# Kernel optimization log

Hardware: AMD Instinct MI355X
Metric: run time of the kernel (lower is better)

The kernel has to match this reference:

```python
import jax, jax.numpy as jnp
import numpy as np

B, S, MAX_K, MID, V = 4, 512, 32, 32, 32000


def _lin(x, W, b):
    # torch nn.Linear convention: W is [out, in]
    return x @ W.T + b


def _label_count_segment(vals):
    """Distinct-label counts over prefixes [0:1],[0:2],...,[0:K] of the kNN labels."""
    Bv, Sv, K = vals.shape
    mask = jnp.triu(jnp.ones((K, K), dtype=bool), k=1)  # [K,K], True above diagonal
    # row i of expand keeps labels [0:i+1], rest filled with -1 (as in masked_fill)
    ev = jnp.where(mask, jnp.array(-1, vals.dtype), vals[:, :, None, :])  # [B,S,K,K]
    s = jnp.sort(ev, axis=-1)
    # zero-out adjacent duplicates (keep first occurrence)
    dedup = jnp.concatenate([s[..., :1], s[..., 1:] * (s[..., 1:] != s[..., :-1])], axis=-1)
    cnt = (dedup != 0).sum(-1)  # [B,S,K]
    cnt = cnt.at[..., :-1].add(-1)  # remove the single surviving -1 for rows 0..K-2
    return cnt


def setup_inputs():
    key = jax.random.key(0)
    ks = jax.random.split(key, 16)
    tgt_index = jax.random.randint(ks[0], (B, S, MAX_K), 0, V)
    knn_dists = jax.random.uniform(ks[1], (B, S, MAX_K), jnp.float32, 1e-3, 10.0)
    knn_key_feature = jax.random.uniform(ks[2], (B, S, MAX_K), jnp.float32, 1e-4, 1.0)
    network_probs = jax.random.uniform(ks[3], (B, S, V), jnp.float32, 1e-6, 1.0)
    network_probs = network_probs / network_probs.sum(-1, keepdims=True)
    network_select_probs = jax.random.uniform(ks[4], (B, S, MAX_K), jnp.float32, 1e-6, 1e-2)
    init = lambda k, shape: 0.02 * jax.random.normal(k, shape, jnp.float32)
    return {
        "tgt_index": tgt_index,
        "knn_dists": knn_dists,
        "knn_key_feature": knn_key_feature,
        "network_probs": network_probs,
        "network_select_probs": network_select_probs,
        # distance_func: Linear(2K+8, 1)
        "W_func": init(ks[5], (1, 2 * MAX_K + 8)), "b_func": init(ks[6], (1,)),
        # distance_fc1: Linear(2,4) -> Tanh -> Linear(4,1)
        "W1a": init(ks[7], (4, 2)), "b1a": init(ks[8], (4,)),
        "W1b": init(ks[9], (1, 4)), "b1b": init(ks[10], (1,)),
        # distance_fc2: Linear(2K, mid) -> Tanh -> Linear(mid, 2)
        "W2a": init(ks[11], (MID, 2 * MAX_K)), "b2a": init(ks[12], (MID,)),
        "W2b": init(ks[13], (2, MID)), "b2b": init(ks[14], (2,)),
    }


def reference(tgt_index, knn_dists, knn_key_feature, network_probs, network_select_probs,
              W_func, b_func, W1a, b1a, W1b, b1b, W2a, b2a, W2b, b2b):
    Bv, Sv, K = knn_dists.shape
    Vv = network_probs.shape[-1]
    label_counts = _label_count_segment(tgt_index)  # [B,S,K] int
    log_key = jnp.log(knn_key_feature)
    log_sel = jnp.log(network_select_probs)
    all_key_feature = jnp.stack([log_key, log_sel], axis=-1)  # [B,S,K,2]
    top_prob, _ = jax.lax.top_k(network_probs, 8)  # [B,S,8]
    knn_feat = jnp.concatenate([knn_dists, label_counts.astype(knn_dists.dtype)], -1)  # [B,S,2K]
    noise_logit = _lin(jnp.tanh(_lin(all_key_feature, W1a, b1a)), W1b, b1b).squeeze(-1)  # [B,S,K]
    sim_in = jnp.concatenate([jnp.log(top_prob), log_key, log_sel], -1)  # [B,S,2K+8]
    sim_lambda = _lin(sim_in, W_func, b_func)  # [B,S,1]
    lambda_logit = _lin(jnp.tanh(_lin(knn_feat, W2a, b2a)), W2b, b2b)  # [B,S,2]
    knn_lambda = jax.nn.softmax(jnp.concatenate([lambda_logit[..., :1], sim_lambda], -1), -1)[..., :1]
    tempe = jax.nn.sigmoid(lambda_logit[..., 1:2])  # [B,S,1]
    probs = jax.nn.softmax(-knn_dists * tempe + noise_logit, -1)  # [B,S,K]
    bi = jnp.arange(Bv)[:, None, None]
    si = jnp.arange(Sv)[None, :, None]
    knn_prob = jnp.zeros((Bv, Sv, Vv), probs.dtype).at[bi, si, tgt_index].set(probs)
    return knn_prob, knn_lambda
```

## Files before the change

### kernel.cpp

```cpp
#include <hip/hip_runtime.h>

typedef unsigned long long ull;
typedef float f4 __attribute__((ext_vector_type(4)));

#define TOKENS 2048
#define KNN    32
#define VOCAB  32000
#define CAP    512

#define INSK(key) do {                                                       \
    ull k_ = (key);                                                          \
    if (k_ > c7) {                                                           \
        ull tmp_;                                                            \
        if (k_ > c0) { tmp_ = c0; c0 = k_; k_ = tmp_; }                      \
        if (k_ > c1) { tmp_ = c1; c1 = k_; k_ = tmp_; }                      \
        if (k_ > c2) { tmp_ = c2; c2 = k_; k_ = tmp_; }                      \
        if (k_ > c3) { tmp_ = c3; c3 = k_; k_ = tmp_; }                      \
        if (k_ > c4) { tmp_ = c4; c4 = k_; k_ = tmp_; }                      \
        if (k_ > c5) { tmp_ = c5; c5 = k_; k_ = tmp_; }                      \
        if (k_ > c6) { tmp_ = c6; c6 = k_; k_ = tmp_; }                      \
        c7 = (k_ > c7) ? k_ : c7;                                            \
    }                                                                        \
} while (0)

#define INSF(vv) do {                                                        \
    float x_ = (vv);                                                         \
    if (x_ > t7) {                                                           \
        float h_;                                                            \
        h_ = fmaxf(t0, x_); x_ = fminf(t0, x_); t0 = h_;                     \
        h_ = fmaxf(t1, x_); x_ = fminf(t1, x_); t1 = h_;                     \
        h_ = fmaxf(t2, x_); x_ = fminf(t2, x_); t2 = h_;                     \
        h_ = fmaxf(t3, x_); x_ = fminf(t3, x_); t3 = h_;                     \
        h_ = fmaxf(t4, x_); x_ = fminf(t4, x_); t4 = h_;                     \
        h_ = fmaxf(t5, x_); x_ = fminf(t5, x_); t5 = h_;                     \
        h_ = fmaxf(t6, x_); x_ = fminf(t6, x_); t6 = h_;                     \
        t7 = fmaxf(t7, x_);                                                  \
    }                                                                        \
} while (0)

#define MAX4(v_) fmaxf(fmaxf(v_.x, v_.y), fmaxf(v_.z, v_.w))

#define COLLECT(v_) do {                                                     \
    if (v_.x >= T) { int p = atomicAdd(&s_n, 1); if (p < CAP) s_cand[p] = v_.x; } \
    if (v_.y >= T) { int p = atomicAdd(&s_n, 1); if (p < CAP) s_cand[p] = v_.y; } \
    if (v_.z >= T) { int p = atomicAdd(&s_n, 1); if (p < CAP) s_cand[p] = v_.z; } \
    if (v_.w >= T) { int p = atomicAdd(&s_n, 1); if (p < CAP) s_cand[p] = v_.w; } \
} while (0)

#define BATCH8(kb) do {                                                      \
    f4 v0 = np4[tid + (((kb)+0) << 8)];                                      \
    f4 v1 = np4[tid + (((kb)+1) << 8)];                                      \
    f4 v2 = np4[tid + (((kb)+2) << 8)];                                      \
    f4 v3 = np4[tid + (((kb)+3) << 8)];                                      \
    f4 v4 = np4[tid + (((kb)+4) << 8)];                                      \
    f4 v5 = np4[tid + (((kb)+5) << 8)];                                      \
    f4 v6 = np4[tid + (((kb)+6) << 8)];                                      \
    f4 v7 = np4[tid + (((kb)+7) << 8)];                                      \
    float m01 = fmaxf(MAX4(v0), MAX4(v1));                                   \
    float m23 = fmaxf(MAX4(v2), MAX4(v3));                                   \
    float m45 = fmaxf(MAX4(v4), MAX4(v5));                                   \
    float m67 = fmaxf(MAX4(v6), MAX4(v7));                                   \
    m = fmaxf(m, fmaxf(fmaxf(m01, m23), fmaxf(m45, m67)));                   \
} while (0)

__global__ __launch_bounds__(256, 8)
void k_scan(const float* __restrict__ net_probs, float* __restrict__ ws)
{
    const int t   = blockIdx.x;
    const int tid = threadIdx.x;

    __shared__ float s_max[256];
    __shared__ float s_cand[CAP];
    __shared__ int   s_n;
    __shared__ float s_thr;
    __shared__ float s_top8[8];

    if (tid == 0) s_n = 0;

    const f4* np4 = (const f4*)(net_probs + (size_t)t * VOCAB);

    float m = 0.f;
    BATCH8(0);
    BATCH8(8);
    BATCH8(16);
    {
        f4 v0 = np4[tid + (24 << 8)];
        f4 v1 = np4[tid + (25 << 8)];
        f4 v2 = np4[tid + (26 << 8)];
        f4 v3 = np4[tid + (27 << 8)];
        f4 v4 = np4[tid + (28 << 8)];
        f4 v5 = np4[tid + (29 << 8)];
        f4 v6 = np4[tid + (30 << 8)];
        float m01 = fmaxf(MAX4(v0), MAX4(v1));
        float m23 = fmaxf(MAX4(v2), MAX4(v3));
        float m45 = fmaxf(MAX4(v4), MAX4(v5));
        m = fmaxf(m, fmaxf(fmaxf(m01, m23), fmaxf(m45, MAX4(v6))));
    }
    if (tid < 64) {
        f4 v = np4[tid + (31 << 8)];
        m = fmaxf(m, MAX4(v));
    }
    s_max[tid] = m;
    __syncthreads();

    if (tid < 64) {
        ull c0 = 0, c1 = 0, c2 = 0, c3 = 0, c4 = 0, c5 = 0, c6 = 0, c7 = 0;
        #pragma unroll
        for (int k = 0; k < 4; ++k) {
            int idx = tid + (k << 6);
            ull key = (((ull)__float_as_uint(s_max[idx])) << 32) | (unsigned)idx;
            INSK(key);
        }
        ull g = 0;
        for (int r = 0; r < 8; ++r) {
            g = c0;
            #pragma unroll
            for (int off = 1; off < 64; off <<= 1) {
                ull o = __shfl_xor(g, off);
                if (o > g) g = o;
            }
            if (c0 == g) {
                c0 = c1; c1 = c2; c2 = c3; c3 = c4; c4 = c5; c5 = c6; c6 = c7; c7 = 0;
            }
        }
        if (tid == 0) s_thr = __uint_as_float((unsigned)(g >> 32));
    }
    __syncthreads();
    const float T = s_thr;

    if (m >= T) {
        for (int k = 0; k < 31; ++k) {
            f4 v = np4[tid + (k << 8)];
            COLLECT(v);
        }
        if (tid < 64) {
            f4 v = np4[tid + (31 << 8)];
            COLLECT(v);
        }
    }
    __syncthreads();
    const int n = s_n;

    if (n <= CAP) {
        if (tid < 64) {
            ull c0 = 0, c1 = 0, c2 = 0, c3 = 0, c4 = 0, c5 = 0, c6 = 0, c7 = 0;
            for (int i = tid; i < n; i += 64) {
                ull key = (((ull)__float_as_uint(s_cand[i])) << 32) | (unsigned)i;
                INSK(key);
            }
            for (int r = 0; r < 8; ++r) {
                ull g = c0;
                #pragma unroll
                for (int off = 1; off < 64; off <<= 1) {
                    ull o = __shfl_xor(g, off);
                    if (o > g) g = o;
                }
                if (c0 == g && g != 0ULL) {
                    c0 = c1; c1 = c2; c2 = c3; c3 = c4; c4 = c5; c5 = c6; c6 = c7; c7 = 0;
                }
                if (tid == 0) s_top8[r] = __uint_as_float((unsigned)(g >> 32));
            }
        }
    } else {
        float t0 = 0.f, t1 = 0.f, t2 = 0.f, t3 = 0.f,
              t4 = 0.f, t5 = 0.f, t6 = 0.f, t7 = 0.f;
        for (int k = 0; k < 31; ++k) {
            f4 v = np4[tid + (k << 8)];
            if (MAX4(v) > t7) { INSF(v.x); INSF(v.y); INSF(v.z); INSF(v.w); }
        }
        if (tid < 64) {
            f4 v = np4[tid + (31 << 8)];
            if (MAX4(v) > t7) { INSF(v.x); INSF(v.y); INSF(v.z); INSF(v.w); }
        }
        for (int r = 0; r < 8; ++r) {
            s_max[tid] = t0;
            __syncthreads();
            if (tid < 64) {
                float g = s_max[tid];
                g = fmaxf(g, s_max[tid + 64]);
                g = fmaxf(g, s_max[tid + 128]);
                g = fmaxf(g, s_max[tid + 192]);
                #pragma unroll
                for (int off = 1; off < 64; off <<= 1)
                    g = fmaxf(g, __shfl_xor(g, off));
                if (tid == 0) { s_thr = g; s_top8[r] = g; }
            }
            __syncthreads();
            float g = s_thr;
            ull mask = __ballot(t0 == g);
            __shared__ int s_win;
            if (tid == 0) s_win = 0x7fffffff;
            __syncthreads();
            if (t0 == g) atomicMin(&s_win, tid);
            __syncthreads();
            if (tid == s_win) {
                t0 = t1; t1 = t2; t2 = t3; t3 = t4; t4 = t5; t5 = t6; t6 = t7; t7 = 0.f;
            }
            __syncthreads();
            (void)mask;
        }
    }
    __syncthreads();

    if (tid < 8) ws[(size_t)t * 8 + tid] = s_top8[tid];
}

__global__ __launch_bounds__(256, 8)
void k_zero(float* __restrict__ out)
{
    const int t   = blockIdx.x;
    const int tid = threadIdx.x;
    f4*      o4 = (f4*)(out + (size_t)t * VOCAB);
    const f4 z4 = (f4){0.f, 0.f, 0.f, 0.f};
    #pragma unroll
    for (int k = 0; k < 31; ++k) o4[tid + (k << 8)] = z4;
    if (tid < 64) o4[tid + (31 << 8)] = z4;
}

__global__ __launch_bounds__(256, 8)
void k2_final(const int*   __restrict__ tgt_index,
              const float* __restrict__ knn_dists,
              const float* __restrict__ knn_key,
              const float* __restrict__ net_sel,
              const float* __restrict__ W_func, const float* __restrict__ b_func,
              const float* __restrict__ W1a,    const float* __restrict__ b1a,
              const float* __restrict__ W1b,    const float* __restrict__ b1b,
              const float* __restrict__ W2a,    const float* __restrict__ b2a,
              const float* __restrict__ W2b,    const float* __restrict__ b2b,
              const float* __restrict__ ws,
              float* __restrict__ out)
{
    const int t   = blockIdx.x;
    const int tid = threadIdx.x;

    __shared__ int   s_tgt[KNN];
    __shared__ float s_dist[KNN];
    __shared__ float s_cnt[KNN];
    __shared__ float s_top8[8];

    int   tg = 0;
    float d = 0.f, lk = 0.f, ls = 0.f;
    if (tid < KNN) {
        tg = tgt_index[t * KNN + tid];
        d  = knn_dists[t * KNN + tid];
        lk = logf(knn_key[t * KNN + tid]);
        ls = logf(net_sel[t * KNN + tid]);
        s_tgt[tid]  = tg;
        s_dist[tid] = d;
    }
    if (tid < 8) s_top8[tid] = ws[(size_t)t * 8 + tid];
    __syncthreads();

    if (tid < KNN) {
        int fo = (tg != 0) ? 1 : 0;
        if (fo) {
            for (int j = 0; j < tid; ++j)
                if (s_tgt[j] == tg) { fo = 0; break; }
        }
        int c = fo;
        #pragma unroll
        for (int off = 1; off < KNN; off <<= 1) {
            int n2 = __shfl_up(c, off, KNN);
            if (tid >= off) c += n2;
        }
        s_cnt[tid] = (float)c;
    }
    __syncthreads();

    if (tid < KNN) {
        float noise = b1b[0];
        #pragma unroll
        for (int j = 0; j < 4; ++j) {
            float z = tanhf(W1a[2 * j] * lk + W1a[2 * j + 1] * ls + b1a[j]);
            noise += W1b[j] * z;
        }

        float sp = W_func[8 + tid] * lk + W_func[40 + tid] * ls;
        if (tid < 8) sp += W_func[tid] * logf(s_top8[tid]);
        #pragma unroll
        for (int off = 16; off; off >>= 1) sp += __shfl_xor(sp, off, KNN);
        float sim = sp + b_func[0];

        float h = b2a[tid];
        const float* wr = W2a + tid * 64;
        #pragma unroll 8
        for (int i = 0; i < KNN; ++i) h += wr[i] * s_dist[i];
        #pragma unroll 8
        for (int i = 0; i < KNN; ++i) h += wr[KNN + i] * s_cnt[i];
        h = tanhf(h);
        float p0 = W2b[tid] * h;
        float p1 = W2b[KNN + tid] * h;
        #pragma unroll
        for (int off = 16; off; off >>= 1) {
            p0 += __shfl_xor(p0, off, KNN);
            p1 += __shfl_xor(p1, off, KNN);
        }
        float l0 = p0 + b2b[0];
        float l1 = p1 + b2b[1];

        float tempe = 1.f / (1.f + expf(-l1));
        float lam   = 1.f / (1.f + expf(-(l0 - sim)));

        float logit = -d * tempe + noise;
        float mx = logit;
        #pragma unroll
        for (int off = 16; off; off >>= 1) mx = fmaxf(mx, __shfl_xor(mx, off, KNN));
        float e = expf(logit - mx);
        float se = e;
        #pragma unroll
        for (int off = 16; off; off >>= 1) se += __shfl_xor(se, off, KNN);
        float p = e / se;

        bool wrte = true;
        for (int j = tid + 1; j < KNN; ++j)
            if (s_tgt[j] == tg) { wrte = false; break; }
        if (wrte) out[(size_t)t * VOCAB + tg] = p;

        if (tid == 0) out[(size_t)TOKENS * VOCAB + t] = lam;
    }
}

extern "C" void kernel_launch(void* const* d_in, const int* in_sizes, int n_in,
                              void* d_out, int out_size, void* d_ws, size_t ws_size,
                              hipStream_t stream) {
    float* ws = (float*)d_ws;

    k_scan<<<TOKENS, 256, 0, stream>>>((const float*)d_in[3], ws);
    k_zero<<<TOKENS, 256, 0, stream>>>((float*)d_out);
    k2_final<<<TOKENS, 256, 0, stream>>>(
        (const int*)  d_in[0],
        (const float*)d_in[1],
        (const float*)d_in[2],
        (const float*)d_in[4],
        (const float*)d_in[5],  (const float*)d_in[6],
        (const float*)d_in[7],  (const float*)d_in[8],
        (const float*)d_in[9],  (const float*)d_in[10],
        (const float*)d_in[11], (const float*)d_in[12],
        (const float*)d_in[13], (const float*)d_in[14],
        ws,
        (float*)d_out);
}
```

Baseline: 147.1 us.

## Split top-8 into flat segment-max pass and fused candidate gather in final kernel

The per-token scan kernel is replaced by a flat streaming kernel that computes the max of each 256-float segment (one wavefront, 125 segments per token) and writes those to the workspace. The top-8 selection then moves into the final kernel: it derives a threshold from the top segment maxima, re-reads only the qualifying segments, and collects candidates in shared memory. The zero-fill kernel also becomes a flat grid-stride pattern. This removes the full second per-token pass and the separate top-k kernel, at the cost of heavier shared-memory use in the final kernel and a dependence on exact segment-to-token alignment.

```diff
diff --git a/kernel.cpp b/kernel.cpp
--- a/kernel.cpp
+++ b/kernel.cpp
@@ -6,7 +6,14 @@
 #define TOKENS 2048
 #define KNN    32
 #define VOCAB  32000
-#define CAP    512
+#define NB_STREAM 2000
+#define NT_STREAM (NB_STREAM * 256)
+#define ITER      32
+#define NWAVE     (NT_STREAM / 64)
+#define SEG_PER_TOK 125
+#define CAP    2048
+
+#define MAX4(v_) fmaxf(fmaxf(v_.x, v_.y), fmaxf(v_.z, v_.w))
 
 #define INSK(key) do {                                                       \
     ull k_ = (key);                                                          \
@@ -38,8 +45,6 @@
     }                                                                        \
 } while (0)
 
-#define MAX4(v_) fmaxf(fmaxf(v_.x, v_.y), fmaxf(v_.z, v_.w))
-
 #define COLLECT(v_) do {                                                     \
     if (v_.x >= T) { int p = atomicAdd(&s_n, 1); if (p < CAP) s_cand[p] = v_.x; } \
     if (v_.y >= T) { int p = atomicAdd(&s_n, 1); if (p < CAP) s_cand[p] = v_.y; } \
@@ -47,70 +52,84 @@
     if (v_.w >= T) { int p = atomicAdd(&s_n, 1); if (p < CAP) s_cand[p] = v_.w; } \
 } while (0)
 
-#define BATCH8(kb) do {                                                      \
-    f4 v0 = np4[tid + (((kb)+0) << 8)];                                      \
-    f4 v1 = np4[tid + (((kb)+1) << 8)];                                      \
-    f4 v2 = np4[tid + (((kb)+2) << 8)];                                      \
-    f4 v3 = np4[tid + (((kb)+3) << 8)];                                      \
-    f4 v4 = np4[tid + (((kb)+4) << 8)];                                      \
-    f4 v5 = np4[tid + (((kb)+5) << 8)];                                      \
-    f4 v6 = np4[tid + (((kb)+6) << 8)];                                      \
-    f4 v7 = np4[tid + (((kb)+7) << 8)];                                      \
-    float m01 = fmaxf(MAX4(v0), MAX4(v1));                                   \
-    float m23 = fmaxf(MAX4(v2), MAX4(v3));                                   \
-    float m45 = fmaxf(MAX4(v4), MAX4(v5));                                   \
-    float m67 = fmaxf(MAX4(v6), MAX4(v7));                                   \
-    m = fmaxf(m, fmaxf(fmaxf(m01, m23), fmaxf(m45, m67)));                   \
-} while (0)
-
 __global__ __launch_bounds__(256, 8)
-void k_scan(const float* __restrict__ net_probs, float* __restrict__ ws)
+void k1_segmax(const float* __restrict__ net_probs, float* __restrict__ ws)
+{
+    const int g = blockIdx.x * 256 + threadIdx.x;
+    const int w = g >> 6;
+    const f4* np4 = (const f4*)net_probs;
+    #pragma unroll 4
+    for (int i = 0; i < ITER; ++i) {
+        f4 v = np4[(size_t)g + (size_t)i * NT_STREAM];
+        float m = MAX4(v);
+        #pragma unroll
+        for (int off = 32; off; off >>= 1) m = fmaxf(m, __shfl_xor(m, off));
+        if ((threadIdx.x & 63) == 0) ws[w + i * NWAVE] = m;
+    }
+}
+
+__global__ __launch_bounds__(256, 8)
+void k_zero(float* __restrict__ out)
+{
+    const int g = blockIdx.x * 256 + threadIdx.x;
+    f4* o4 = (f4*)out;
+    const f4 z4 = (f4){0.f, 0.f, 0.f, 0.f};
+    #pragma unroll 8
+    for (int i = 0; i < ITER; ++i)
+        o4[(size_t)g + (size_t)i * NT_STREAM] = z4;
+}
+
+__global__ __launch_bounds__(256, 8)
+void k2_final(const int*   __restrict__ tgt_index,
+              const float* __restrict__ knn_dists,
+              const float* __restrict__ knn_key,
+              const float* __restrict__ net_probs,
+              const float* __restrict__ net_sel,
+              const float* __restrict__ W_func, const float* __restrict__ b_func,
+              const float* __restrict__ W1a,    const float* __restrict__ b1a,
+              const float* __restrict__ W1b,    const float* __restrict__ b1b,
+              const float* __restrict__ W2a,    const float* __restrict__ b2a,
+              const float* __restrict__ W2b,    const float* __restrict__ b2b,
+              const float* __restrict__ ws,
+              float* __restrict__ out)
 {
     const int t   = blockIdx.x;
     const int tid = threadIdx.x;
 
-    __shared__ float s_max[256];
+    __shared__ float s_sm[128];
+    __shared__ int   s_qseg[128];
+    __shared__ int   s_nq;
+    __shared__ float s_thr;
     __shared__ float s_cand[CAP];
     __shared__ int   s_n;
-    __shared__ float s_thr;
+    __shared__ float s_red[256];
+    __shared__ int   s_win;
+    __shared__ int   s_tgt[KNN];
+    __shared__ float s_dist[KNN];
+    __shared__ float s_cnt[KNN];
     __shared__ float s_top8[8];
 
-    if (tid == 0) s_n = 0;
-
-    const f4* np4 = (const f4*)(net_probs + (size_t)t * VOCAB);
-
-    float m = 0.f;
-    BATCH8(0);
-    BATCH8(8);
-    BATCH8(16);
-    {
-        f4 v0 = np4[tid + (24 << 8)];
-        f4 v1 = np4[tid + (25 << 8)];
-        f4 v2 = np4[tid + (26 << 8)];
-        f4 v3 = np4[tid + (27 << 8)];
-        f4 v4 = np4[tid + (28 << 8)];
-        f4 v5 = np4[tid + (29 << 8)];
-        f4 v6 = np4[tid + (30 << 8)];
-        float m01 = fmaxf(MAX4(v0), MAX4(v1));
-        float m23 = fmaxf(MAX4(v2), MAX4(v3));
-        float m45 = fmaxf(MAX4(v4), MAX4(v5));
-        m = fmaxf(m, fmaxf(fmaxf(m01, m23), fmaxf(m45, MAX4(v6))));
-    }
-    if (tid < 64) {
-        f4 v = np4[tid + (31 << 8)];
-        m = fmaxf(m, MAX4(v));
-    }
-    s_max[tid] = m;
+    if (tid == 0) { s_nq = 0; s_n = 0; }
+
+    int   tg = 0;
+    float d = 0.f, lk = 0.f, ls = 0.f;
+    if (tid < KNN) {
+        tg = tgt_index[t * KNN + tid];
+        d  = knn_dists[t * KNN + tid];
+        lk = logf(knn_key[t * KNN + tid]);
+        ls = logf(net_sel[t * KNN + tid]);
+        s_tgt[tid]  = tg;
+        s_dist[tid] = d;
+    }
+    if (tid < 128) s_sm[tid] = (tid < SEG_PER_TOK) ? ws[t * SEG_PER_TOK + tid] : 0.f;
     __syncthreads();
 
     if (tid < 64) {
         ull c0 = 0, c1 = 0, c2 = 0, c3 = 0, c4 = 0, c5 = 0, c6 = 0, c7 = 0;
-        #pragma unroll
-        for (int k = 0; k < 4; ++k) {
-            int idx = tid + (k << 6);
-            ull key = (((ull)__float_as_uint(s_max[idx])) << 32) | (unsigned)idx;
-            INSK(key);
-        }
+        ull k0 = (((ull)__float_as_uint(s_sm[tid])) << 32) | (unsigned)tid;
+        INSK(k0);
+        ull k1 = (((ull)__float_as_uint(s_sm[tid + 64])) << 32) | (unsigned)(tid + 64);
+        INSK(k1);
         ull g = 0;
         for (int r = 0; r < 8; ++r) {
             g = c0;
@@ -128,13 +147,19 @@
     __syncthreads();
     const float T = s_thr;
 
-    if (m >= T) {
-        for (int k = 0; k < 31; ++k) {
-            f4 v = np4[tid + (k << 8)];
-            COLLECT(v);
-        }
-        if (tid < 64) {
-            f4 v = np4[tid + (31 << 8)];
+    if (tid < SEG_PER_TOK && s_sm[tid] >= T) {
+        int p = atomicAdd(&s_nq, 1);
+        s_qseg[p] = tid;
+    }
+    __syncthreads();
+    const int nq = s_nq;
+
+    const f4* np4 = (const f4*)(net_probs + (size_t)t * VOCAB);
+    for (int base = 0; base < nq; base += 4) {
+        int qi = base + (tid >> 6);
+        if (qi < nq) {
+            int seg = s_qseg[qi];
+            f4 v = np4[seg * 64 + (tid & 63)];
             COLLECT(v);
         }
     }
@@ -173,82 +198,28 @@
             if (MAX4(v) > t7) { INSF(v.x); INSF(v.y); INSF(v.z); INSF(v.w); }
         }
         for (int r = 0; r < 8; ++r) {
-            s_max[tid] = t0;
+            s_red[tid] = t0;
             __syncthreads();
             if (tid < 64) {
-                float g = s_max[tid];
-                g = fmaxf(g, s_max[tid + 64]);
-                g = fmaxf(g, s_max[tid + 128]);
-                g = fmaxf(g, s_max[tid + 192]);
+                float g = s_red[tid];
+                g = fmaxf(g, s_red[tid + 64]);
+                g = fmaxf(g, s_red[tid + 128]);
+                g = fmaxf(g, s_red[tid + 192]);
                 #pragma unroll
                 for (int off = 1; off < 64; off <<= 1)
                     g = fmaxf(g, __shfl_xor(g, off));
                 if (tid == 0) { s_thr = g; s_top8[r] = g; }
             }
-            __syncthreads();
-            float g = s_thr;
-            ull mask = __ballot(t0 == g);
-            __shared__ int s_win;
             if (tid == 0) s_win = 0x7fffffff;
             __syncthreads();
-            if (t0 == g) atomicMin(&s_win, tid);
+            if (t0 == s_thr) atomicMin(&s_win, tid);
             __syncthreads();
             if (tid == s_win) {
                 t0 = t1; t1 = t2; t2 = t3; t3 = t4; t4 = t5; t5 = t6; t6 = t7; t7 = 0.f;
             }
             __syncthreads();
-            (void)mask;
-        }
-    }
-    __syncthreads();
-
-    if (tid < 8) ws[(size_t)t * 8 + tid] = s_top8[tid];
-}
-
-__global__ __launch_bounds__(256, 8)
-void k_zero(float* __restrict__ out)
-{
-    const int t   = blockIdx.x;
-    const int tid = threadIdx.x;
-    f4*      o4 = (f4*)(out + (size_t)t * VOCAB);
-    const f4 z4 = (f4){0.f, 0.f, 0.f, 0.f};
-    #pragma unroll
-    for (int k = 0; k < 31; ++k) o4[tid + (k << 8)] = z4;
-    if (tid < 64) o4[tid + (31 << 8)] = z4;
-}
-
-__global__ __launch_bounds__(256, 8)
-void k2_final(const int*   __restrict__ tgt_index,
-              const float* __restrict__ knn_dists,
-              const float* __restrict__ knn_key,
-              const float* __restrict__ net_sel,
-              const float* __restrict__ W_func, const float* __restrict__ b_func,
-              const float* __restrict__ W1a,    const float* __restrict__ b1a,
-              const float* __restrict__ W1b,    const float* __restrict__ b1b,
-              const float* __restrict__ W2a,    const float* __restrict__ b2a,
-              const float* __restrict__ W2b,    const float* __restrict__ b2b,
-              const float* __restrict__ ws,
-              float* __restrict__ out)
-{
-    const int t   = blockIdx.x;
-    const int tid = threadIdx.x;
-
-    __shared__ int   s_tgt[KNN];
-    __shared__ float s_dist[KNN];
-    __shared__ float s_cnt[KNN];
-    __shared__ float s_top8[8];
-
-    int   tg = 0;
-    float d = 0.f, lk = 0.f, ls = 0.f;
-    if (tid < KNN) {
-        tg = tgt_index[t * KNN + tid];
-        d  = knn_dists[t * KNN + tid];
-        lk = logf(knn_key[t * KNN + tid]);
-        ls = logf(net_sel[t * KNN + tid]);
-        s_tgt[tid]  = tg;
-        s_dist[tid] = d;
-    }
-    if (tid < 8) s_top8[tid] = ws[(size_t)t * 8 + tid];
+        }
+    }
     __syncthreads();
 
     if (tid < KNN) {
@@ -325,12 +296,13 @@
                               hipStream_t stream) {
     float* ws = (float*)d_ws;
 
-    k_scan<<<TOKENS, 256, 0, stream>>>((const float*)d_in[3], ws);
-    k_zero<<<TOKENS, 256, 0, stream>>>((float*)d_out);
+    k1_segmax<<<NB_STREAM, 256, 0, stream>>>((const float*)d_in[3], ws);
+    k_zero<<<NB_STREAM, 256, 0, stream>>>((float*)d_out);
     k2_final<<<TOKENS, 256, 0, stream>>>(
         (const int*)  d_in[0],
         (const float*)d_in[1],
         (const float*)d_in[2],
+        (const float*)d_in[3],
         (const float*)d_in[4],
         (const float*)d_in[5],  (const float*)d_in[6],
         (const float*)d_in[7],  (const float*)d_in[8],
```

Result: faster. 137.7 us (-6.4%).
